# Optimization experiments

Measured on AMD Instinct MI355X. Metric: run time of the kernel, lower is better.

The kernel has to match this reference:

```python
import jax, jax.numpy as jnp
import numpy as np

BATCH, IN_SIZE, IN_DIM = 64, 4096, 128
HEADS, OUT_SIZE = 2, 128
EPS = 0.1
MAX_ITER = 50


def setup_inputs() -> dict:
    key = jax.random.key(0)
    k1, k2 = jax.random.split(key)
    x = jax.random.normal(k1, (BATCH, IN_SIZE, IN_DIM), dtype=jnp.float32)
    # xavier-normal-like init: std = sqrt(2/(in_dim+out_size)) ~= 0.05 keeps exp(dot/eps) finite
    weight = 0.05 * jax.random.normal(k2, (HEADS, OUT_SIZE, IN_DIM), dtype=jnp.float32)
    return {"x": x, "weight": weight}


def _sinkhorn(K, a, max_iter):
    # K: N x in_size x out_size (Gibbs kernel, all positive)
    # row marginal a = out_size / in_size, column marginal 1 (per OTK's sinkhorn())
    n, in_size, out_size = K.shape
    u0 = jnp.ones((n, in_size), K.dtype)
    v0 = jnp.ones((n, out_size), K.dtype)

    def body(carry, _):
        u, v = carry
        u = a / jnp.einsum('nio,no->ni', K, v)   # u = a / (K v)
        v = 1.0 / jnp.einsum('ni,nio->no', u, K)  # v = 1 / (u^T K)
        return (u, v), None

    (u, v), _ = jax.lax.scan(body, (u0, v0), None, length=max_iter)
    # transport plan T = diag(u) K diag(v)
    return u[:, :, None] * K * v[:, None, :]


def reference(x, weight):
    n, in_size, in_dim = x.shape
    m, out_size, _ = weight.shape
    # dot products between inputs and reference points: n x m x in_size x out_size
    dot = jnp.einsum('nid,mod->nmio', x, weight)
    K = jnp.exp(dot / EPS).reshape(n * m, in_size, out_size)
    T = _sinkhorn(K, out_size / in_size, MAX_ITER)
    T = T.reshape(n, m, in_size, out_size)
    # attn: n x out_size x m x in_size  (== multihead_attn output)
    attn = jnp.transpose(T, (0, 3, 1, 2))
    # bmm(attn.view(n, out*m, in_size), x) -> n x out_size x (m*in_dim)
    out = jnp.einsum('nomi,nid->nomd', attn, x)
    return out.reshape(n, out_size, m * in_dim)
```

## Files before the change

kernel.cpp:

```cpp
#include <hip/hip_runtime.h>
#include <hip/hip_bf16.h>

#define BATCH 64
#define IN_SIZE 4096
#define IN_DIM 128
#define HEADS 2
#define OUT_SIZE 128
#define NPAIR (BATCH*HEADS)
#define NBLK (NPAIR*2)
#define INV_EPS 10.0f
#define MAX_ITER 50
#define A_MARG (1.0f/32.0f)

typedef unsigned int u32;
typedef __attribute__((ext_vector_type(8))) short bf16x8;
typedef __attribute__((ext_vector_type(4))) float f32x4;

__device__ __forceinline__ float bflo(u32 kk){ return __uint_as_float(kk<<16); }
__device__ __forceinline__ float bfhi(u32 kk){ return __uint_as_float(kk & 0xffff0000u); }
__device__ __forceinline__ unsigned short f2bf(float f){
    __hip_bfloat16 h = __float2bfloat16(f);
    return *(unsigned short*)&h;
}

template<int CTRL>
__device__ __forceinline__ float dpp_add(float x) {
    int yi = __builtin_amdgcn_update_dpp(0, __float_as_int(x), CTRL, 0xf, 0xf, false);
    return x + __int_as_float(yi);
}

__global__ __launch_bounds__(256) void kgen(const float* __restrict__ x,
                                            const float* __restrict__ w,
                                            __hip_bfloat16* __restrict__ Kb)
{
    const int pair = blockIdx.y;
    const int n = pair >> 1, m = pair & 1;
    const int r0 = blockIdx.x * 128;
    const int tid = threadIdx.x;
    const int wv  = tid >> 6;
    const int l   = tid & 63;

    __shared__ char xs[128*256];
    __shared__ char ws[128*256];

    {
        const float* xb = x + ((size_t)n*IN_SIZE + r0)*IN_DIM;
        for (int t = tid; t < 4096; t += 256) {
            int row = t >> 5, c4 = t & 31;
            float4 v4 = *(const float4*)&xb[(size_t)row*IN_DIM + c4*4];
            u32 p0 = (u32)f2bf(v4.x) | ((u32)f2bf(v4.y) << 16);
            u32 p1 = (u32)f2bf(v4.z) | ((u32)f2bf(v4.w) << 16);
            int byte = (row*256 + c4*8) ^ ((row & 7) << 4);
            *(u32*)(xs + byte)     = p0;
            *(u32*)(xs + byte + 4) = p1;
        }
    }
    {
        const float* wb = w + (size_t)m*OUT_SIZE*IN_DIM;
        for (int t = tid; t < 4096; t += 256) {
            int row = t >> 5, c4 = t & 31;
            float4 v4 = *(const float4*)&wb[(size_t)row*IN_DIM + c4*4];
            u32 p0 = (u32)f2bf(v4.x) | ((u32)f2bf(v4.y) << 16);
            u32 p1 = (u32)f2bf(v4.z) | ((u32)f2bf(v4.w) << 16);
            int byte = (row*256 + c4*8) ^ ((row & 7) << 4);
            *(u32*)(ws + byte)     = p0;
            *(u32*)(ws + byte + 4) = p1;
        }
    }
    __syncthreads();

    f32x4 acc[2][8];
    #pragma unroll
    for (int ai=0;ai<2;++ai)
        #pragma unroll
        for (int bj=0;bj<8;++bj) acc[ai][bj] = (f32x4){0.f,0.f,0.f,0.f};

    const int lr = l & 15;
    const int lk = (l >> 4) * 16;

    #pragma unroll
    for (int kk = 0; kk < 4; ++kk) {
        bf16x8 a[2];
        #pragma unroll
        for (int ai=0;ai<2;++ai) {
            int row = wv*32 + ai*16 + lr;
            int byte = (row*256 + kk*64 + lk) ^ ((row & 7) << 4);
            a[ai] = *(const bf16x8*)(xs + byte);
        }
        #pragma unroll
        for (int bj=0;bj<8;++bj) {
            int row = bj*16 + lr;
            int byte = (row*256 + kk*64 + lk) ^ ((row & 7) << 4);
            bf16x8 b = *(const bf16x8*)(ws + byte);
            acc[0][bj] = __builtin_amdgcn_mfma_f32_16x16x32_bf16(a[0], b, acc[0][bj], 0, 0, 0);
            acc[1][bj] = __builtin_amdgcn_mfma_f32_16x16x32_bf16(a[1], b, acc[1][bj], 0, 0, 0);
        }
    }

    __hip_bfloat16* out = Kb + (size_t)pair*IN_SIZE*OUT_SIZE + (size_t)r0*OUT_SIZE;
    #pragma unroll
    for (int ai=0;ai<2;++ai) {
        #pragma unroll
        for (int bj=0;bj<8;++bj) {
            #pragma unroll
            for (int j=0;j<4;++j) {
                int i = wv*32 + ai*16 + (l>>4)*4 + j;
                int o = bj*16 + lr;
                float e = __expf(INV_EPS * acc[ai][bj][j]);
                out[(size_t)i*OUT_SIZE + o] = __float2bfloat16(e);
            }
        }
    }
}

__global__ __launch_bounds__(1024) void sinkhorn(const __hip_bfloat16* __restrict__ Kb,
                                                 float* __restrict__ uo,
                                                 float* __restrict__ vo,
                                                 int* __restrict__ slots)
{
    const int bid  = blockIdx.x;
    const int pair = bid >> 1, half = bid & 1;
    const int tid  = threadIdx.x;
    const int wave = tid >> 6;
    const int lane = tid & 63;
    const int grp  = lane >> 4;
    const int s    = lane & 15;

    __shared__ float red[16][128];
    __shared__ float vnew[128];

    const int4* gp = (const int4*)(Kb)
                   + ((size_t)pair*4096 + half*2048 + wave*128)*16
                   + grp*16 + s;

    float v[8];
    #pragma unroll
    for (int j=0;j<8;++j) v[j] = 1.f;

    for (int it = 0; it < MAX_ITER; ++it) {
        const bool last = (it == MAX_ITER-1);
        float acc[8];
        #pragma unroll
        for (int j=0;j<8;++j) acc[j] = 0.f;

        int4 c0 = gp[0], c1 = gp[64], c2 = gp[128], c3 = gp[192];
        for (int g = 0; g < 32; ++g) {
            int gn = g + 4; if (gn > 31) gn = 31;
            int4 nx = gp[(size_t)gn*64];
            float k[8];
            k[0]=bflo(c0.x); k[1]=bfhi(c0.x);
            k[2]=bflo(c0.y); k[3]=bfhi(c0.y);
            k[4]=bflo(c0.z); k[5]=bfhi(c0.z);
            k[6]=bflo(c0.w); k[7]=bfhi(c0.w);
            float p = k[0]*v[0];
            #pragma unroll
            for (int j=1;j<8;++j) p = fmaf(k[j], v[j], p);
            p = dpp_add<0xB1>(p);
            p = dpp_add<0x4E>(p);
            p = dpp_add<0x141>(p);
            p = dpp_add<0x140>(p);
            float ui = A_MARG * __builtin_amdgcn_rcpf(p);
            #pragma unroll
            for (int j=0;j<8;++j) acc[j] = fmaf(ui, k[j], acc[j]);
            if (last && s == 0)
                uo[(size_t)pair*IN_SIZE + half*2048 + wave*128 + g*4 + grp] = ui;
            c0 = c1; c1 = c2; c2 = c3; c3 = nx;
        }
        #pragma unroll
        for (int j=0;j<8;++j) {
            acc[j] += __shfl_xor(acc[j], 16, 64);
            acc[j] += __shfl_xor(acc[j], 32, 64);
        }
        if (lane < 16) {
            *(float4*)&red[wave][8*s]   = make_float4(acc[0],acc[1],acc[2],acc[3]);
            *(float4*)&red[wave][8*s+4] = make_float4(acc[4],acc[5],acc[6],acc[7]);
        }
        __syncthreads();
        if (tid < 128) {
            float own = 0.f;
            #pragma unroll
            for (int w_ = 0; w_ < 16; ++w_) own += red[w_][tid];
            int* myslot = slots + ((size_t)it*NBLK + bid)*128;
            int* otslot = slots + ((size_t)it*NBLK + (bid^1))*128;
            __hip_atomic_store(&myslot[tid], __float_as_int(-own),
                               __ATOMIC_RELAXED, __HIP_MEMORY_SCOPE_AGENT);
            int wrd;
            do {
                wrd = __hip_atomic_load(&otslot[tid], __ATOMIC_RELAXED,
                                        __HIP_MEMORY_SCOPE_AGENT);
            } while (wrd >= 0);
            float other = -__int_as_float(wrd);
            float vv = __builtin_amdgcn_rcpf(own + other);
            vnew[tid] = vv;
            if (last && half == 0) vo[(size_t)pair*OUT_SIZE + tid] = vv;
        }
        __syncthreads();
        float4 va = *(const float4*)&vnew[8*s];
        float4 vb = *(const float4*)&vnew[8*s+4];
        v[0]=va.x; v[1]=va.y; v[2]=va.z; v[3]=va.w;
        v[4]=vb.x; v[5]=vb.y; v[6]=vb.z; v[7]=vb.w;
    }
}

__global__ __launch_bounds__(256) void outgemm(const __hip_bfloat16* __restrict__ Kb,
                                               const float* __restrict__ uo,
                                               const float* __restrict__ vo,
                                               const float* __restrict__ x,
                                               float* __restrict__ out)
{
    const int dh = blockIdx.x;
    const int pair = blockIdx.y;
    const int n = pair >> 1, m = pair & 1;
    const int tid = threadIdx.x;
    const int wv  = tid >> 6;
    const int l   = tid & 63;

    __shared__ u32  ka[64][66];
    __shared__ float ua[64];
    __shared__ float xa[64][68];
    __shared__ char At[128*128];
    __shared__ char Bt[64*128];

    f32x4 acc[2][4];
    #pragma unroll
    for (int ai=0;ai<2;++ai)
        #pragma unroll
        for (int bj=0;bj<4;++bj) acc[ai][bj] = (f32x4){0.f,0.f,0.f,0.f};

    const int lr = l & 15;
    const int lk = (l >> 4) * 16;

    for (int chunk = 0; chunk < 64; ++chunk) {
        const int i0 = chunk * 64;
        {
            const u32* ksrc = (const u32*)(Kb + ((size_t)pair*IN_SIZE + i0)*OUT_SIZE);
            for (int t = tid; t < 4096; t += 256) ka[t>>6][t&63] = ksrc[t];
            if (tid < 64) ua[tid] = uo[(size_t)pair*IN_SIZE + i0 + tid];
            const float* xsrc = x + ((size_t)n*IN_SIZE + i0)*IN_DIM + dh*64;
            for (int t = tid; t < 1024; t += 256) {
                int i = t >> 4, c4 = t & 15;
                *(float4*)&xa[i][c4*4] = *(const float4*)&xsrc[(size_t)i*IN_DIM + c4*4];
            }
        }
        __syncthreads();
        {
            int o = tid >> 1, seg = tid & 1;
            unsigned short us[32];
            #pragma unroll
            for (int k=0;k<32;++k) {
                int i = seg*32 + k;
                u32 kk = ka[i][o>>1];
                float f = (o&1) ? bfhi(kk) : bflo(kk);
                us[k] = f2bf(f * ua[i]);
            }
            #pragma unroll
            for (int q=0;q<4;++q) {
                int4 wbuf;
                u32* wp = (u32*)&wbuf;
                #pragma unroll
                for (int e=0;e<4;++e)
                    wp[e] = (u32)us[q*8 + 2*e] | ((u32)us[q*8 + 2*e + 1] << 16);
                int byte = (o*128 + seg*64 + q*16) ^ ((o & 7) << 4);
                *(int4*)(At + byte) = wbuf;
            }
        }
        {
            int d = tid >> 2, s2 = tid & 3;
            unsigned short us[16];
            #pragma unroll
            for (int k=0;k<16;++k) us[k] = f2bf(xa[s2*16 + k][d]);
            #pragma unroll
            for (int q=0;q<2;++q) {
                int4 wbuf;
                u32* wp = (u32*)&wbuf;
                #pragma unroll
                for (int e=0;e<4;++e)
                    wp[e] = (u32)us[q*8 + 2*e] | ((u32)us[q*8 + 2*e + 1] << 16);
                int byte = (d*128 + s2*32 + q*16) ^ ((d & 7) << 4);
                *(int4*)(Bt + byte) = wbuf;
            }
        }
        __syncthreads();
        #pragma unroll
        for (int kk = 0; kk < 2; ++kk) {
            bf16x8 a[2];
            #pragma unroll
            for (int ai=0;ai<2;++ai) {
                int row = wv*32 + ai*16 + lr;
                int byte = (row*128 + kk*64 + lk) ^ ((row & 7) << 4);
                a[ai] = *(const bf16x8*)(At + byte);
            }
            #pragma unroll
            for (int bj=0;bj<4;++bj) {
                int row = bj*16 + lr;
                int byte = (row*128 + kk*64 + lk) ^ ((row & 7) << 4);
                bf16x8 b = *(const bf16x8*)(Bt + byte);
                acc[0][bj] = __builtin_amdgcn_mfma_f32_16x16x32_bf16(a[0], b, acc[0][bj], 0, 0, 0);
                acc[1][bj] = __builtin_amdgcn_mfma_f32_16x16x32_bf16(a[1], b, acc[1][bj], 0, 0, 0);
            }
        }
        __syncthreads();
    }

    #pragma unroll
    for (int ai=0;ai<2;++ai) {
        #pragma unroll
        for (int bj=0;bj<4;++bj) {
            #pragma unroll
            for (int j=0;j<4;++j) {
                int o = wv*32 + ai*16 + (l>>4)*4 + j;
                int d = dh*64 + bj*16 + lr;
                float vv = vo[(size_t)pair*OUT_SIZE + o];
                out[(((size_t)n*OUT_SIZE + o)*HEADS + m)*IN_DIM + d] = acc[ai][bj][j] * vv;
            }
        }
    }
}

extern "C" void kernel_launch(void* const* d_in, const int* in_sizes, int n_in,
                              void* d_out, int out_size, void* d_ws, size_t ws_size,
                              hipStream_t stream)
{
    const float* x = (const float*)d_in[0];
    const float* w = (const float*)d_in[1];
    float* out = (float*)d_out;

    char* ws = (char*)d_ws;
    __hip_bfloat16* Kb = (__hip_bfloat16*)ws;
    float* uo  = (float*)(ws + 134217728);
    float* vo  = (float*)(ws + 134217728 + 2097152);
    int* slots = (int*)(ws + 134217728 + 2097152 + 65536);

    hipMemsetAsync(slots, 0, (size_t)MAX_ITER*NBLK*128*sizeof(int), stream);

    kgen    <<<dim3(IN_SIZE/128, NPAIR), 256,  0, stream>>>(x, w, Kb);
    sinkhorn<<<dim3(NBLK),               1024, 0, stream>>>(Kb, uo, vo, slots);
    outgemm <<<dim3(2, NPAIR),           256,  0, stream>>>(Kb, uo, vo, x, out);
}
```

Before: 1.521 ms.

## Cache Sinkhorn kernel tile in registers and LDS across iterations

```diff
diff --git a/kernel.cpp b/kernel.cpp
--- a/kernel.cpp
+++ b/kernel.cpp
@@ -113,10 +113,30 @@
     }
 }
 
-__global__ __launch_bounds__(1024) void sinkhorn(const __hip_bfloat16* __restrict__ Kb,
-                                                 float* __restrict__ uo,
-                                                 float* __restrict__ vo,
-                                                 int* __restrict__ slots)
+#define PROC_QUAD(cc, qidx)                                                   \
+    {                                                                         \
+        float k0=bflo((cc).x), k1=bfhi((cc).x), k2=bflo((cc).y), k3=bfhi((cc).y); \
+        float k4=bflo((cc).z), k5=bfhi((cc).z), k6=bflo((cc).w), k7=bfhi((cc).w); \
+        float p = k0*v[0];                                                    \
+        p = fmaf(k1,v[1],p); p = fmaf(k2,v[2],p); p = fmaf(k3,v[3],p);        \
+        p = fmaf(k4,v[4],p); p = fmaf(k5,v[5],p); p = fmaf(k6,v[6],p);        \
+        p = fmaf(k7,v[7],p);                                                  \
+        p = dpp_add<0xB1>(p);                                                 \
+        p = dpp_add<0x4E>(p);                                                 \
+        p = dpp_add<0x141>(p);                                                \
+        p = dpp_add<0x140>(p);                                                \
+        float ui = A_MARG * __builtin_amdgcn_rcpf(p);                         \
+        acc[0]=fmaf(ui,k0,acc[0]); acc[1]=fmaf(ui,k1,acc[1]);                 \
+        acc[2]=fmaf(ui,k2,acc[2]); acc[3]=fmaf(ui,k3,acc[3]);                 \
+        acc[4]=fmaf(ui,k4,acc[4]); acc[5]=fmaf(ui,k5,acc[5]);                 \
+        acc[6]=fmaf(ui,k6,acc[6]); acc[7]=fmaf(ui,k7,acc[7]);                 \
+        if (last && s == 0) uo[uob + (qidx)*4 + grp] = ui;                    \
+    }
+
+__global__ __launch_bounds__(1024, 4) void sinkhorn(const __hip_bfloat16* __restrict__ Kb,
+                                                    float* __restrict__ uo,
+                                                    float* __restrict__ vo,
+                                                    int* __restrict__ slots)
 {
     const int bid  = blockIdx.x;
     const int pair = bid >> 1, half = bid & 1;
@@ -126,16 +146,30 @@
     const int grp  = lane >> 4;
     const int s    = lane & 15;
 
+    __shared__ int4  klds[16*8*64];
     __shared__ float red[16][128];
     __shared__ float vnew[128];
 
     const int4* gp = (const int4*)(Kb)
                    + ((size_t)pair*4096 + half*2048 + wave*128)*16
                    + grp*16 + s;
+    const size_t uob = (size_t)pair*IN_SIZE + half*2048 + wave*128;
+
+    int4 kq0  = gp[ 0*64], kq1  = gp[ 1*64], kq2  = gp[ 2*64], kq3  = gp[ 3*64];
+    int4 kq4  = gp[ 4*64], kq5  = gp[ 5*64], kq6  = gp[ 6*64], kq7  = gp[ 7*64];
+    int4 kq8  = gp[ 8*64], kq9  = gp[ 9*64], kq10 = gp[10*64], kq11 = gp[11*64];
+    int4 kq12 = gp[12*64], kq13 = gp[13*64], kq14 = gp[14*64], kq15 = gp[15*64];
+    #pragma unroll
+    for (int q = 0; q < 8; ++q)
+        klds[(wave*8 + q)*64 + lane] = gp[(16+q)*64];
+
+    const int4* sp = gp + 24*64;
 
     float v[8];
     #pragma unroll
     for (int j=0;j<8;++j) v[j] = 1.f;
+
+    int4 c0 = sp[0*64], c1 = sp[1*64], c2 = sp[2*64], c3 = sp[3*64];
 
     for (int it = 0; it < MAX_ITER; ++it) {
         const bool last = (it == MAX_ITER-1);
@@ -143,29 +177,24 @@
         #pragma unroll
         for (int j=0;j<8;++j) acc[j] = 0.f;
 
-        int4 c0 = gp[0], c1 = gp[64], c2 = gp[128], c3 = gp[192];
-        for (int g = 0; g < 32; ++g) {
-            int gn = g + 4; if (gn > 31) gn = 31;
-            int4 nx = gp[(size_t)gn*64];
-            float k[8];
-            k[0]=bflo(c0.x); k[1]=bfhi(c0.x);
-            k[2]=bflo(c0.y); k[3]=bfhi(c0.y);
-            k[4]=bflo(c0.z); k[5]=bfhi(c0.z);
-            k[6]=bflo(c0.w); k[7]=bfhi(c0.w);
-            float p = k[0]*v[0];
-            #pragma unroll
-            for (int j=1;j<8;++j) p = fmaf(k[j], v[j], p);
-            p = dpp_add<0xB1>(p);
-            p = dpp_add<0x4E>(p);
-            p = dpp_add<0x141>(p);
-            p = dpp_add<0x140>(p);
-            float ui = A_MARG * __builtin_amdgcn_rcpf(p);
-            #pragma unroll
-            for (int j=0;j<8;++j) acc[j] = fmaf(ui, k[j], acc[j]);
-            if (last && s == 0)
-                uo[(size_t)pair*IN_SIZE + half*2048 + wave*128 + g*4 + grp] = ui;
+        PROC_QUAD(kq0,  0)  PROC_QUAD(kq1,  1)  PROC_QUAD(kq2,  2)  PROC_QUAD(kq3,  3)
+        PROC_QUAD(kq4,  4)  PROC_QUAD(kq5,  5)  PROC_QUAD(kq6,  6)  PROC_QUAD(kq7,  7)
+        PROC_QUAD(kq8,  8)  PROC_QUAD(kq9,  9)  PROC_QUAD(kq10,10)  PROC_QUAD(kq11,11)
+        PROC_QUAD(kq12,12)  PROC_QUAD(kq13,13)  PROC_QUAD(kq14,14)  PROC_QUAD(kq15,15)
+
+        #pragma unroll
+        for (int q = 0; q < 8; ++q) {
+            int4 cc = klds[(wave*8 + q)*64 + lane];
+            PROC_QUAD(cc, 16+q)
+        }
+
+        #pragma unroll
+        for (int g = 0; g < 8; ++g) {
+            int4 nx = sp[(size_t)((g+4)&7)*64];
+            PROC_QUAD(c0, 24+g)
             c0 = c1; c1 = c2; c2 = c3; c3 = nx;
         }
+
         #pragma unroll
         for (int j=0;j<8;++j) {
             acc[j] += __shfl_xor(acc[j], 16, 64);
```

Result: slower. 4.653 ms (+206.0%).
